# Performance work log

Hardware: AMD Instinct MI355X
Metric: run time of the kernel (lower is better)

Reference implementation:

```python
import jax, jax.numpy as jnp
import numpy as np

HIDDEN = 128
EDGE_DIM = 64
N_NODES = 50000
N_EDGES = 600000

def _linear_params(key, fan_in, fan_out):
    kw, kb = jax.random.split(key)
    bound = 1.0 / np.sqrt(fan_in)
    W = jax.random.uniform(kw, (fan_in, fan_out), minval=-bound, maxval=bound, dtype=jnp.float32)
    b = jax.random.uniform(kb, (fan_out,), minval=-bound, maxval=bound, dtype=jnp.float32)
    return W, b

def setup_inputs() -> dict:
    key = jax.random.key(0)
    ks = jax.random.split(key, 10)
    h = jax.random.normal(ks[0], (N_NODES, HIDDEN), dtype=jnp.float32)
    edge_index = jax.random.randint(ks[1], (2, N_EDGES), 0, N_NODES, dtype=jnp.int64)
    edge_attr = jax.random.normal(ks[2], (N_EDGES, EDGE_DIM), dtype=jnp.float32)
    mW1, mb1 = _linear_params(ks[3], 2 * HIDDEN + EDGE_DIM, HIDDEN)
    mW2, mb2 = _linear_params(ks[4], HIDDEN, HIDDEN)
    mW3, mb3 = _linear_params(ks[5], HIDDEN, HIDDEN)
    uW1, ub1 = _linear_params(ks[6], 2 * HIDDEN, HIDDEN)
    uW2, ub2 = _linear_params(ks[7], HIDDEN, HIDDEN)
    gamma = jnp.ones((HIDDEN,), dtype=jnp.float32)
    beta = jnp.zeros((HIDDEN,), dtype=jnp.float32)
    return {"h": h, "edge_index": edge_index, "edge_attr": edge_attr,
            "mW1": mW1, "mb1": mb1, "mW2": mW2, "mb2": mb2, "mW3": mW3, "mb3": mb3,
            "uW1": uW1, "ub1": ub1, "uW2": uW2, "ub2": ub2,
            "gamma": gamma, "beta": beta}

def reference(h, edge_index, edge_attr, mW1, mb1, mW2, mb2, mW3, mb3, uW1, ub1, uW2, ub2, gamma, beta):
    src, dst = edge_index[0], edge_index[1]
    # message MLP on [E, 2*H + edge_dim]
    x = jnp.concatenate([h[src], h[dst], edge_attr], axis=-1)
    x = jax.nn.gelu(x @ mW1 + mb1)
    x = jax.nn.gelu(x @ mW2 + mb2)
    msgs = x @ mW3 + mb3  # [E, H]
    # scatter-mean aggregate to destination nodes
    agg = jax.ops.segment_sum(msgs, dst, num_segments=h.shape[0])
    count = jax.ops.segment_sum(jnp.ones((dst.shape[0], 1), dtype=h.dtype), dst, num_segments=h.shape[0])
    agg = agg / (count + 1e-8)
    # update MLP
    u = jnp.concatenate([h, agg], axis=-1)
    u = jax.nn.gelu(u @ uW1 + ub1)
    out = u @ uW2 + ub2
    # LayerNorm(out + h)
    y = out + h
    mu = jnp.mean(y, axis=-1, keepdims=True)
    var = jnp.var(y, axis=-1, keepdims=True)
    return (y - mu) / jnp.sqrt(var + 1e-5) * gamma + beta
```

## Files before the change

kernel.cpp:

```cpp
#include <hip/hip_runtime.h>

#define E_TOTAL 600000
#define NN 50000

typedef _Float16 half8 __attribute__((ext_vector_type(8)));
typedef _Float16 half2v __attribute__((ext_vector_type(2)));
typedef float float4v __attribute__((ext_vector_type(4)));
typedef float float2v __attribute__((ext_vector_type(2)));

__device__ __forceinline__ float gelu_tanh(float x) {
    const float A = 1.5957691216057308f;
    const float B = 0.0713548163f;
    float z = x * __builtin_fmaf(B, x * x, A);
    float ex = __expf(z);
    float r = __builtin_amdgcn_rcpf(ex + 1.0f);
    return __builtin_fmaf(-x, r, x);
}

__device__ __forceinline__ int act_idx(int c, int row, int q) {
    int idx = ((c * 128 + row) << 3) + q;
    idx ^= ((row >> 3) & 3) << 4;
    idx ^= (c & 1) << 3;
    return idx;
}
__device__ __forceinline__ int act_idx64(int c, int row, int q) {
    int idx = ((c * 64 + row) << 3) + q;
    idx ^= ((row >> 3) & 3) << 4;
    idx ^= (c & 1) << 3;
    return idx;
}

__device__ __forceinline__ half8 cvt8(float4v x0, float4v x1) {
    half8 a;
    a[0] = (_Float16)x0[0]; a[1] = (_Float16)x0[1]; a[2] = (_Float16)x0[2]; a[3] = (_Float16)x0[3];
    a[4] = (_Float16)x1[0]; a[5] = (_Float16)x1[1]; a[6] = (_Float16)x1[2]; a[7] = (_Float16)x1[3];
    return a;
}

__global__ __launch_bounds__(256) void prep_kernel(
    const float* __restrict__ mW1, const float* __restrict__ mW2, const float* __restrict__ mW3,
    const float* __restrict__ uW1, const float* __restrict__ uW2,
    const float* __restrict__ h,
    _Float16* __restrict__ pw, _Float16* __restrict__ hf)
{
    const int stride = gridDim.x * 256;
    for (int t = blockIdx.x * 256 + threadIdx.x; t < 922880; t += stride) {
        if (t < 122880) {
            const float* src;
            int loc;
            if (t < 40960)        { src = mW1; loc = t; }
            else if (t < 57344)   { src = mW2; loc = t - 40960; }
            else if (t < 73728)   { src = mW3; loc = t - 57344; }
            else if (t < 106496)  { src = uW1; loc = t - 73728; }
            else                  { src = uW2; loc = t - 106496; }
            int i   = loc & 7;
            int col = (loc >> 3) & 127;
            int c   = loc >> 10;
            pw[t] = (_Float16)src[(8 * c + i) * 128 + col];
        } else {
            int i = t - 122880;
            float4v a = ((const float4v*)h)[2 * i];
            float4v b = ((const float4v*)h)[2 * i + 1];
            ((half8*)hf)[i] = cvt8(a, b);
        }
    }
}

__device__ __forceinline__ int detect_i64(const int* ei) {
    int allz = 1;
    #pragma unroll
    for (int j = 1; j < 64; j += 2) allz &= (ei[j] == 0);
    return allz;
}

__global__ __launch_bounds__(256) void count_kernel(const int* __restrict__ ei, int* __restrict__ cnt_i) {
    __shared__ int s_mode;
    if (threadIdx.x == 0) s_mode = detect_i64(ei);
    __syncthreads();
    int e = blockIdx.x * 256 + threadIdx.x;
    if (e >= E_TOTAL) return;
    int d = s_mode ? (int)((const long long*)ei)[E_TOTAL + e] : ei[E_TOTAL + e];
    atomicAdd(&cnt_i[d], 1);
}

__global__ __launch_bounds__(1024) void scan_kernel(const int* __restrict__ cnt_i, int* __restrict__ offs) {
    __shared__ int part[1024];
    const int t = threadIdx.x;
    const int PER = (NN + 1023) / 1024;
    const int base = t * PER;
    int s = 0;
    for (int j = 0; j < PER; ++j) { int idx = base + j; if (idx < NN) s += cnt_i[idx]; }
    part[t] = s;
    __syncthreads();
    for (int off = 1; off < 1024; off <<= 1) {
        int v = (t >= off) ? part[t - off] : 0;
        __syncthreads();
        part[t] += v;
        __syncthreads();
    }
    int run = (t == 0) ? 0 : part[t - 1];
    for (int j = 0; j < PER; ++j) { int idx = base + j; if (idx < NN) { offs[idx] = run; run += cnt_i[idx]; } }
    if (t == 1023) offs[NN] = part[1023];
}

__global__ __launch_bounds__(256) void fill_kernel(const int* __restrict__ ei, const int* __restrict__ offs,
                                                   int* __restrict__ cursor, int* __restrict__ perm) {
    __shared__ int s_mode;
    if (threadIdx.x == 0) s_mode = detect_i64(ei);
    __syncthreads();
    int e = blockIdx.x * 256 + threadIdx.x;
    if (e >= E_TOTAL) return;
    int d = s_mode ? (int)((const long long*)ei)[E_TOTAL + e] : ei[E_TOTAL + e];
    int pos = offs[d] + atomicAdd(&cursor[d], 1);
    perm[pos] = e;
}

template<int ATOMIC>
__global__ __launch_bounds__(128, 3) void msg_kernel(
    const _Float16* __restrict__ hf16, const int* __restrict__ ei, const float* __restrict__ eattr,
    const int* __restrict__ perm,
    const _Float16* __restrict__ pw1, const _Float16* __restrict__ pw2, const _Float16* __restrict__ pw3,
    const float* __restrict__ mb1, const float* __restrict__ mb2, const float* __restrict__ mb3,
    _Float16* __restrict__ msgs, float* __restrict__ agg, float* __restrict__ cnt)
{
    __shared__ int s_e[64];
    __shared__ int s_src[64];
    __shared__ int s_dst[64];
    __shared__ int s_mode;
    __shared__ __align__(16) _Float16 s_act[16 * 64 * 8];

    const int tid = threadIdx.x;
    const int e0  = blockIdx.x * 64;

    if (tid == 0) s_mode = detect_i64(ei);
    __syncthreads();

    if (tid < 64) {
        int e = perm[e0 + tid];
        s_e[tid] = e;
        int srcn, dstn;
        if (s_mode) {
            const long long* e64 = (const long long*)ei;
            srcn = (int)e64[e];
            dstn = (int)e64[E_TOTAL + e];
        } else {
            srcn = ei[e];
            dstn = ei[E_TOTAL + e];
        }
        s_src[tid] = srcn;
        s_dst[tid] = dstn;
        if (ATOMIC) unsafeAtomicAdd(&cnt[dstn], 1.0f);
    }
    __syncthreads();

    const int w = tid >> 6, l = tid & 63, lhi = l >> 4, llo = l & 15;
    const int r0 = 32 * w;
    const float4v fzero = {0.0f, 0.0f, 0.0f, 0.0f};

    const _Float16* srcP[2];
    const _Float16* dstP[2];
    const float*    eP[2];
    #pragma unroll
    for (int ms = 0; ms < 2; ++ms) {
        const int row = r0 + 16 * ms + llo;
        srcP[ms] = hf16 + (size_t)s_src[row] * 128 + 8 * lhi;
        dstP[ms] = hf16 + (size_t)s_dst[row] * 128 + 8 * lhi;
        eP[ms]   = eattr + (size_t)s_e[row] * 64 + 8 * lhi;
    }

    float4v acc[2][8];
    #pragma unroll
    for (int ms = 0; ms < 2; ++ms)
        #pragma unroll
        for (int t = 0; t < 8; ++t) acc[ms][t] = fzero;

    half8 af[4][2];
    #pragma unroll
    for (int s = 0; s < 4; ++s)
        #pragma unroll
        for (int ms = 0; ms < 2; ++ms)
            af[s][ms] = *(const half8*)(srcP[ms] + 32 * s);

    #pragma unroll
    for (int s = 0; s < 10; ++s) {
        const int bbase = ((4 * s + lhi) * 128 + llo) << 3;
        #pragma unroll
        for (int t = 0; t < 8; ++t) {
            const half8 b = *(const half8*)(pw1 + bbase + (t << 7));
            acc[0][t] = __builtin_amdgcn_mfma_f32_16x16x32_f16(af[s & 3][0], b, acc[0][t], 0, 0, 0);
            acc[1][t] = __builtin_amdgcn_mfma_f32_16x16x32_f16(af[s & 3][1], b, acc[1][t], 0, 0, 0);
        }
        if (s + 4 <= 9) {
            const int sn = s + 4;
            #pragma unroll
            for (int ms = 0; ms < 2; ++ms) {
                if (sn < 8) {
                    af[sn & 3][ms] = *(const half8*)(dstP[ms] + 32 * (sn - 4));
                } else {
                    const float* p = eP[ms] + 32 * (sn - 8);
                    float4v x0 = *(const float4v*)p;
                    float4v x1 = *(const float4v*)(p + 4);
                    af[sn & 3][ms] = cvt8(x0, x1);
                }
            }
        }
    }

    #pragma unroll
    for (int t = 0; t < 8; ++t) {
        const int col = 16 * t + llo;
        const float b1 = mb1[col];
        #pragma unroll
        for (int ms = 0; ms < 2; ++ms)
            #pragma unroll
            for (int i = 0; i < 4; ++i) {
                const int row = r0 + 16 * ms + 4 * lhi + i;
                float v = gelu_tanh(acc[ms][t][i] + b1);
                s_act[act_idx64(col >> 3, row, col & 7)] = (_Float16)v;
            }
    }

    float4v acc2[2][8];
    #pragma unroll
    for (int ms = 0; ms < 2; ++ms)
        #pragma unroll
        for (int t = 0; t < 8; ++t) acc2[ms][t] = fzero;

    #pragma unroll
    for (int s = 0; s < 4; ++s) {
        half8 a2[2];
        #pragma unroll
        for (int ms = 0; ms < 2; ++ms)
            a2[ms] = *(const half8*)&s_act[act_idx64(4 * s + lhi, r0 + 16 * ms + llo, 0)];
        const int bbase = ((4 * s + lhi) * 128 + llo) << 3;
        #pragma unroll
        for (int t = 0; t < 8; ++t) {
            const half8 b = *(const half8*)(pw2 + bbase + (t << 7));
            acc2[0][t] = __builtin_amdgcn_mfma_f32_16x16x32_f16(a2[0], b, acc2[0][t], 0, 0, 0);
            acc2[1][t] = __builtin_amdgcn_mfma_f32_16x16x32_f16(a2[1], b, acc2[1][t], 0, 0, 0);
        }
    }

    #pragma unroll
    for (int t = 0; t < 8; ++t) {
        const int col = 16 * t + llo;
        const float b2 = mb2[col];
        #pragma unroll
        for (int ms = 0; ms < 2; ++ms)
            #pragma unroll
            for (int i = 0; i < 4; ++i) {
                const int row = r0 + 16 * ms + 4 * lhi + i;
                float v = gelu_tanh(acc2[ms][t][i] + b2);
                s_act[act_idx64(col >> 3, row, col & 7)] = (_Float16)v;
            }
    }

    float4v acc3[2][8];
    #pragma unroll
    for (int ms = 0; ms < 2; ++ms)
        #pragma unroll
        for (int t = 0; t < 8; ++t) acc3[ms][t] = fzero;

    #pragma unroll
    for (int s = 0; s < 4; ++s) {
        half8 a3[2];
        #pragma unroll
        for (int ms = 0; ms < 2; ++ms)
            a3[ms] = *(const half8*)&s_act[act_idx64(4 * s + lhi, r0 + 16 * ms + llo, 0)];
        const int bbase = ((4 * s + lhi) * 128 + llo) << 3;
        #pragma unroll
        for (int t = 0; t < 8; ++t) {
            const half8 b = *(const half8*)(pw3 + bbase + (t << 7));
            acc3[0][t] = __builtin_amdgcn_mfma_f32_16x16x32_f16(a3[0], b, acc3[0][t], 0, 0, 0);
            acc3[1][t] = __builtin_amdgcn_mfma_f32_16x16x32_f16(a3[1], b, acc3[1][t], 0, 0, 0);
        }
    }

    float mb3v[8];
    #pragma unroll
    for (int t = 0; t < 8; ++t) mb3v[t] = mb3[16 * t + llo];

    #pragma unroll
    for (int ms = 0; ms < 2; ++ms)
        #pragma unroll
        for (int i = 0; i < 4; ++i) {
            const int row = r0 + 16 * ms + 4 * lhi + i;
            if (ATOMIC) {
                const size_t dbase = (size_t)s_dst[row] * 128;
                #pragma unroll
                for (int t = 0; t < 8; ++t)
                    unsafeAtomicAdd(&agg[dbase + 16 * t + llo], acc3[ms][t][i] + mb3v[t]);
            } else {
                _Float16* mrow = msgs + (size_t)(e0 + row) * 128;
                #pragma unroll
                for (int t = 0; t < 8; ++t)
                    __builtin_nontemporal_store((_Float16)(acc3[ms][t][i] + mb3v[t]), mrow + 16 * t + llo);
            }
        }
}

template<int FUSED>
__global__ __launch_bounds__(256) void upd_kernel(
    const float* __restrict__ h, const _Float16* __restrict__ hf16,
    const _Float16* __restrict__ msgs, const int* __restrict__ offs,
    const _Float16* __restrict__ pu1, const _Float16* __restrict__ pu2,
    const float* __restrict__ ub1, const float* __restrict__ ub2,
    const float* __restrict__ gamma, const float* __restrict__ beta,
    const float* __restrict__ agg, const float* __restrict__ cnt,
    float* __restrict__ out)
{
    __shared__ __align__(16) _Float16 s_act[16 * 128 * 8];

    const int tid = threadIdx.x;
    const int n0  = blockIdx.x * 128;
    const int w = tid >> 6, l = tid & 63, lhi = l >> 4, llo = l & 15;
    const int r0 = 32 * w;
    const float4v fzero = {0.0f, 0.0f, 0.0f, 0.0f};

    float rcp[2];
    size_t nodeOff[2];
    int beg[2], end[2];
    #pragma unroll
    for (int ms = 0; ms < 2; ++ms) {
        int node = n0 + r0 + 16 * ms + llo;
        if (node >= NN) node = NN - 1;
        nodeOff[ms] = (size_t)node * 128;
        if (FUSED) {
            beg[ms] = offs[node]; end[ms] = offs[node + 1];
            rcp[ms] = 1.0f / ((float)(end[ms] - beg[ms]) + 1e-8f);
        } else {
            rcp[ms] = 1.0f / (cnt[node] + 1e-8f);
        }
    }

    half8 afA[2][4];
    if (FUSED) {
        #pragma unroll
        for (int ms = 0; ms < 2; ++ms) {
            float msum[4][8];
            #pragma unroll
            for (int s = 0; s < 4; ++s)
                #pragma unroll
                for (int j = 0; j < 8; ++j) msum[s][j] = 0.0f;
            for (int r = beg[ms]; r < end[ms]; ++r) {
                const half8* rp = (const half8*)(msgs + (size_t)r * 128) + lhi;
                #pragma unroll
                for (int s = 0; s < 4; ++s) {
                    half8 v = __builtin_nontemporal_load(rp + 4 * s);
                    #pragma unroll
                    for (int j = 0; j < 8; ++j) msum[s][j] += (float)v[j];
                }
            }
            #pragma unroll
            for (int s = 0; s < 4; ++s) {
                half8 a;
                #pragma unroll
                for (int j = 0; j < 8; ++j) a[j] = (_Float16)(msum[s][j] * rcp[ms]);
                afA[ms][s] = a;
            }
        }
    }

    float4v acc[2][8];
    #pragma unroll
    for (int ms = 0; ms < 2; ++ms)
        #pragma unroll
        for (int t = 0; t < 8; ++t) acc[ms][t] = fzero;

    #pragma unroll
    for (int s = 0; s < 8; ++s) {
        half8 af[2];
        #pragma unroll
        for (int ms = 0; ms < 2; ++ms) {
            if (s < 4) {
                af[ms] = *(const half8*)(hf16 + nodeOff[ms] + 32 * s + 8 * lhi);
            } else if (FUSED) {
                af[ms] = afA[ms][s - 4];
            } else {
                const float* p = agg + nodeOff[ms] + 32 * (s - 4) + 8 * lhi;
                float4v x0 = *(const float4v*)p;
                float4v x1 = *(const float4v*)(p + 4);
                x0 *= rcp[ms]; x1 *= rcp[ms];
                af[ms] = cvt8(x0, x1);
            }
        }
        const int bbase = ((4 * s + lhi) * 128 + llo) << 3;
        #pragma unroll
        for (int t = 0; t < 8; ++t) {
            const half8 b = *(const half8*)(pu1 + bbase + (t << 7));
            acc[0][t] = __builtin_amdgcn_mfma_f32_16x16x32_f16(af[0], b, acc[0][t], 0, 0, 0);
            acc[1][t] = __builtin_amdgcn_mfma_f32_16x16x32_f16(af[1], b, acc[1][t], 0, 0, 0);
        }
    }

    #pragma unroll
    for (int t = 0; t < 8; ++t) {
        const int col = 16 * t + llo;
        const float b1 = ub1[col];
        #pragma unroll
        for (int ms = 0; ms < 2; ++ms)
            #pragma unroll
            for (int i = 0; i < 4; ++i) {
                const int row = r0 + 16 * ms + 4 * lhi + i;
                float v = gelu_tanh(acc[ms][t][i] + b1);
                s_act[act_idx(col >> 3, row, col & 7)] = (_Float16)v;
            }
    }

    float4v acc2[2][8];
    #pragma unroll
    for (int ms = 0; ms < 2; ++ms)
        #pragma unroll
        for (int t = 0; t < 8; ++t) acc2[ms][t] = fzero;

    #pragma unroll
    for (int s = 0; s < 4; ++s) {
        half8 af[2];
        #pragma unroll
        for (int ms = 0; ms < 2; ++ms)
            af[ms] = *(const half8*)&s_act[act_idx(4 * s + lhi, r0 + 16 * ms + llo, 0)];
        const int bbase = ((4 * s + lhi) * 128 + llo) << 3;
        #pragma unroll
        for (int t = 0; t < 8; ++t) {
            const half8 b = *(const half8*)(pu2 + bbase + (t << 7));
            acc2[0][t] = __builtin_amdgcn_mfma_f32_16x16x32_f16(af[0], b, acc2[0][t], 0, 0, 0);
            acc2[1][t] = __builtin_amdgcn_mfma_f32_16x16x32_f16(af[1], b, acc2[1][t], 0, 0, 0);
        }
    }

    float ub2v[8], gv[8], bv[8];
    #pragma unroll
    for (int t = 0; t < 8; ++t) {
        const int col = 16 * t + llo;
        ub2v[t] = ub2[col]; gv[t] = gamma[col]; bv[t] = beta[col];
    }

    #pragma unroll
    for (int ms = 0; ms < 2; ++ms)
        #pragma unroll
        for (int i = 0; i < 4; ++i) {
            const int noderow = n0 + r0 + 16 * ms + 4 * lhi + i;
            const int nodec = noderow < NN ? noderow : NN - 1;
            float y[8];
            float sum = 0.0f;
            #pragma unroll
            for (int t = 0; t < 8; ++t) {
                const int col = 16 * t + llo;
                float v = acc2[ms][t][i] + ub2v[t] + h[(size_t)nodec * 128 + col];
                y[t] = v; sum += v;
            }
            sum += __shfl_xor(sum, 1, 16);
            sum += __shfl_xor(sum, 2, 16);
            sum += __shfl_xor(sum, 4, 16);
            sum += __shfl_xor(sum, 8, 16);
            const float mu = sum * (1.0f / 128.0f);
            float sq = 0.0f;
            #pragma unroll
            for (int t = 0; t < 8; ++t) { float d = y[t] - mu; sq += d * d; }
            sq += __shfl_xor(sq, 1, 16);
            sq += __shfl_xor(sq, 2, 16);
            sq += __shfl_xor(sq, 4, 16);
            sq += __shfl_xor(sq, 8, 16);
            const float rs = rsqrtf(sq * (1.0f / 128.0f) + 1e-5f);
            if (noderow < NN) {
                #pragma unroll
                for (int t = 0; t < 8; ++t) {
                    const int col = 16 * t + llo;
                    out[(size_t)noderow * 128 + col] = (y[t] - mu) * rs * gv[t] + bv[t];
                }
            }
        }
}

extern "C" void kernel_launch(void* const* d_in, const int* in_sizes, int n_in,
                              void* d_out, int out_size, void* d_ws, size_t ws_size,
                              hipStream_t stream) {
    const float* h     = (const float*)d_in[0];
    const int*   ei    = (const int*)d_in[1];
    const float* eattr = (const float*)d_in[2];
    const float* mW1   = (const float*)d_in[3];
    const float* mb1   = (const float*)d_in[4];
    const float* mW2   = (const float*)d_in[5];
    const float* mb2   = (const float*)d_in[6];
    const float* mW3   = (const float*)d_in[7];
    const float* mb3   = (const float*)d_in[8];
    const float* uW1   = (const float*)d_in[9];
    const float* ub1   = (const float*)d_in[10];
    const float* uW2   = (const float*)d_in[11];
    const float* ub2   = (const float*)d_in[12];
    const float* gamma = (const float*)d_in[13];
    const float* beta  = (const float*)d_in[14];
    float* out = (float*)d_out;

    char* ws = (char*)d_ws;

    const size_t OFF_MSGS = 0;
    const size_t OFF_HF   = 153600000;
    const size_t OFF_CNTI = 166400000;
    const size_t OFF_CURS = 166600000;
    const size_t OFF_OFFS = 166800000;
    const size_t OFF_PERM = 167000064;
    const size_t OFF_PW   = 169400064;
    const size_t NEED     = 169645824;

    if (ws_size >= NEED) {
        _Float16* msgs  = (_Float16*)(ws + OFF_MSGS);
        _Float16* hf16  = (_Float16*)(ws + OFF_HF);
        int* cnt_i      = (int*)(ws + OFF_CNTI);
        int* cursor     = (int*)(ws + OFF_CURS);
        int* offs       = (int*)(ws + OFF_OFFS);
        int* perm       = (int*)(ws + OFF_PERM);
        _Float16* pw    = (_Float16*)(ws + OFF_PW);
        _Float16* pw1 = pw;
        _Float16* pw2 = pw + 40960;
        _Float16* pw3 = pw + 57344;
        _Float16* pu1 = pw + 73728;
        _Float16* pu2 = pw + 106496;

        hipMemsetAsync(ws + OFF_CNTI, 0, 400000, stream);

        count_kernel<<<(E_TOTAL + 255) / 256, 256, 0, stream>>>(ei, cnt_i);
        scan_kernel<<<1, 1024, 0, stream>>>(cnt_i, offs);
        fill_kernel<<<(E_TOTAL + 255) / 256, 256, 0, stream>>>(ei, offs, cursor, perm);
        prep_kernel<<<1024, 256, 0, stream>>>(mW1, mW2, mW3, uW1, uW2, h, pw, hf16);

        msg_kernel<0><<<E_TOTAL / 64, 128, 0, stream>>>(
            hf16, ei, eattr, perm, pw1, pw2, pw3, mb1, mb2, mb3, msgs, nullptr, nullptr);

        upd_kernel<1><<<(NN + 127) / 128, 256, 0, stream>>>(
            h, hf16, msgs, offs, pu1, pu2, ub1, ub2, gamma, beta, nullptr, nullptr, out);
    } else {
        float* agg     = (float*)ws;
        float* cnt     = (float*)(ws + 25600000);
        _Float16* hf16 = (_Float16*)(ws + 25800000);
        int* cnt_i     = (int*)(ws + 38600000);
        int* cursor    = (int*)(ws + 38800000);
        int* offs      = (int*)(ws + 39000000);
        int* perm      = (int*)(ws + 39200064);
        _Float16* pw   = (_Float16*)(ws + 41600064);
        _Float16* pw1 = pw;
        _Float16* pw2 = pw + 40960;
        _Float16* pw3 = pw + 57344;
        _Float16* pu1 = pw + 73728;
        _Float16* pu2 = pw + 106496;

        hipMemsetAsync(ws, 0, 25800000, stream);
        hipMemsetAsync(ws + 38600000, 0, 400000, stream);

        count_kernel<<<(E_TOTAL + 255) / 256, 256, 0, stream>>>(ei, cnt_i);
        scan_kernel<<<1, 1024, 0, stream>>>(cnt_i, offs);
        fill_kernel<<<(E_TOTAL + 255) / 256, 256, 0, stream>>>(ei, offs, cursor, perm);
        prep_kernel<<<1024, 256, 0, stream>>>(mW1, mW2, mW3, uW1, uW2, h, pw, hf16);

        msg_kernel<1><<<E_TOTAL / 64, 128, 0, stream>>>(
            hf16, ei, eattr, perm, pw1, pw2, pw3, mb1, mb2, mb3, nullptr, agg, cnt);

        upd_kernel<0><<<(NN + 127) / 128, 256, 0, stream>>>(
            h, hf16, nullptr, nullptr, pu1, pu2, ub1, ub2, gamma, beta, agg, cnt, out);
    }
}
```

Measured before the change: 716.6 us.

## Process edges in natural order, scatter messages by rank, add separate aggregation kernel

The message kernel now reads edges in their original order, so edge_attr and edge_index loads are contiguous instead of gathered through a permutation. Each message row is written to its CSR-sorted slot using a rank array built by the fill kernel. A new aggregation kernel, one wavefront per node, sums each node's contiguous message rows into an fp16 mean buffer. The update kernel then just loads that buffer, which removes the serial per-lane reduction loop and its load imbalance. This costs an extra launch and an extra round-trip of the aggregate buffer, and the message stores become scattered. The fallback path drops the unused CSR build.

```diff
diff --git a/kernel.cpp b/kernel.cpp
--- a/kernel.cpp
+++ b/kernel.cpp
@@ -104,7 +104,7 @@
 }
 
 __global__ __launch_bounds__(256) void fill_kernel(const int* __restrict__ ei, const int* __restrict__ offs,
-                                                   int* __restrict__ cursor, int* __restrict__ perm) {
+                                                   int* __restrict__ cursor, int* __restrict__ rank) {
     __shared__ int s_mode;
     if (threadIdx.x == 0) s_mode = detect_i64(ei);
     __syncthreads();
@@ -112,20 +112,46 @@
     if (e >= E_TOTAL) return;
     int d = s_mode ? (int)((const long long*)ei)[E_TOTAL + e] : ei[E_TOTAL + e];
     int pos = offs[d] + atomicAdd(&cursor[d], 1);
-    perm[pos] = e;
+    rank[e] = pos;
+}
+
+__global__ __launch_bounds__(256) void agg_kernel(const _Float16* __restrict__ msgs,
+                                                  const int* __restrict__ offs,
+                                                  _Float16* __restrict__ aggf) {
+    const int node = blockIdx.x * 4 + (threadIdx.x >> 6);
+    const int l = threadIdx.x & 63;
+    const int beg = offs[node], end = offs[node + 1];
+    float2v s = {0.0f, 0.0f};
+    const half2v* p = (const half2v*)msgs + (size_t)beg * 64 + l;
+    int j = beg;
+    for (; j + 3 < end; j += 4, p += 256) {
+        half2v a = __builtin_nontemporal_load(p);
+        half2v b = __builtin_nontemporal_load(p + 64);
+        half2v c = __builtin_nontemporal_load(p + 128);
+        half2v d = __builtin_nontemporal_load(p + 192);
+        s.x += (float)a[0] + (float)b[0] + (float)c[0] + (float)d[0];
+        s.y += (float)a[1] + (float)b[1] + (float)c[1] + (float)d[1];
+    }
+    for (; j < end; ++j, p += 64) {
+        half2v v = __builtin_nontemporal_load(p);
+        s.x += (float)v[0]; s.y += (float)v[1];
+    }
+    const float rcp = 1.0f / ((float)(end - beg) + 1e-8f);
+    half2v o; o[0] = (_Float16)(s.x * rcp); o[1] = (_Float16)(s.y * rcp);
+    ((half2v*)aggf)[(size_t)node * 64 + l] = o;
 }
 
 template<int ATOMIC>
 __global__ __launch_bounds__(128, 3) void msg_kernel(
     const _Float16* __restrict__ hf16, const int* __restrict__ ei, const float* __restrict__ eattr,
-    const int* __restrict__ perm,
+    const int* __restrict__ rank,
     const _Float16* __restrict__ pw1, const _Float16* __restrict__ pw2, const _Float16* __restrict__ pw3,
     const float* __restrict__ mb1, const float* __restrict__ mb2, const float* __restrict__ mb3,
     _Float16* __restrict__ msgs, float* __restrict__ agg, float* __restrict__ cnt)
 {
-    __shared__ int s_e[64];
     __shared__ int s_src[64];
     __shared__ int s_dst[64];
+    __shared__ int s_rk[64];
     __shared__ int s_mode;
     __shared__ __align__(16) _Float16 s_act[16 * 64 * 8];
 
@@ -136,8 +162,7 @@
     __syncthreads();
 
     if (tid < 64) {
-        int e = perm[e0 + tid];
-        s_e[tid] = e;
+        int e = e0 + tid;
         int srcn, dstn;
         if (s_mode) {
             const long long* e64 = (const long long*)ei;
@@ -149,7 +174,11 @@
         }
         s_src[tid] = srcn;
         s_dst[tid] = dstn;
-        if (ATOMIC) unsafeAtomicAdd(&cnt[dstn], 1.0f);
+        if (ATOMIC) {
+            unsafeAtomicAdd(&cnt[dstn], 1.0f);
+        } else {
+            s_rk[tid] = rank[e];
+        }
     }
     __syncthreads();
 
@@ -165,7 +194,7 @@
         const int row = r0 + 16 * ms + llo;
         srcP[ms] = hf16 + (size_t)s_src[row] * 128 + 8 * lhi;
         dstP[ms] = hf16 + (size_t)s_dst[row] * 128 + 8 * lhi;
-        eP[ms]   = eattr + (size_t)s_e[row] * 64 + 8 * lhi;
+        eP[ms]   = eattr + (size_t)(e0 + row) * 64 + 8 * lhi;
     }
 
     float4v acc[2][8];
@@ -291,7 +320,7 @@
                 for (int t = 0; t < 8; ++t)
                     unsafeAtomicAdd(&agg[dbase + 16 * t + llo], acc3[ms][t][i] + mb3v[t]);
             } else {
-                _Float16* mrow = msgs + (size_t)(e0 + row) * 128;
+                _Float16* mrow = msgs + (size_t)s_rk[row] * 128;
                 #pragma unroll
                 for (int t = 0; t < 8; ++t)
                     __builtin_nontemporal_store((_Float16)(acc3[ms][t][i] + mb3v[t]), mrow + 16 * t + llo);
@@ -299,10 +328,10 @@
         }
 }
 
-template<int FUSED>
+template<int AGGF16>
 __global__ __launch_bounds__(256) void upd_kernel(
     const float* __restrict__ h, const _Float16* __restrict__ hf16,
-    const _Float16* __restrict__ msgs, const int* __restrict__ offs,
+    const _Float16* __restrict__ aggf,
     const _Float16* __restrict__ pu1, const _Float16* __restrict__ pu2,
     const float* __restrict__ ub1, const float* __restrict__ ub2,
     const float* __restrict__ gamma, const float* __restrict__ beta,
@@ -319,46 +348,12 @@
 
     float rcp[2];
     size_t nodeOff[2];
-    int beg[2], end[2];
     #pragma unroll
     for (int ms = 0; ms < 2; ++ms) {
         int node = n0 + r0 + 16 * ms + llo;
         if (node >= NN) node = NN - 1;
         nodeOff[ms] = (size_t)node * 128;
-        if (FUSED) {
-            beg[ms] = offs[node]; end[ms] = offs[node + 1];
-            rcp[ms] = 1.0f / ((float)(end[ms] - beg[ms]) + 1e-8f);
-        } else {
-            rcp[ms] = 1.0f / (cnt[node] + 1e-8f);
-        }
-    }
-
-    half8 afA[2][4];
-    if (FUSED) {
-        #pragma unroll
-        for (int ms = 0; ms < 2; ++ms) {
-            float msum[4][8];
-            #pragma unroll
-            for (int s = 0; s < 4; ++s)
-                #pragma unroll
-                for (int j = 0; j < 8; ++j) msum[s][j] = 0.0f;
-            for (int r = beg[ms]; r < end[ms]; ++r) {
-                const half8* rp = (const half8*)(msgs + (size_t)r * 128) + lhi;
-                #pragma unroll
-                for (int s = 0; s < 4; ++s) {
-                    half8 v = __builtin_nontemporal_load(rp + 4 * s);
-                    #pragma unroll
-                    for (int j = 0; j < 8; ++j) msum[s][j] += (float)v[j];
-                }
-            }
-            #pragma unroll
-            for (int s = 0; s < 4; ++s) {
-                half8 a;
-                #pragma unroll
-                for (int j = 0; j < 8; ++j) a[j] = (_Float16)(msum[s][j] * rcp[ms]);
-                afA[ms][s] = a;
-            }
-        }
+        if (!AGGF16) rcp[ms] = 1.0f / (cnt[node] + 1e-8f);
     }
 
     float4v acc[2][8];
@@ -374,8 +369,8 @@
         for (int ms = 0; ms < 2; ++ms) {
             if (s < 4) {
                 af[ms] = *(const half8*)(hf16 + nodeOff[ms] + 32 * s + 8 * lhi);
-            } else if (FUSED) {
-                af[ms] = afA[ms][s - 4];
+            } else if (AGGF16) {
+                af[ms] = *(const half8*)(aggf + nodeOff[ms] + 32 * (s - 4) + 8 * lhi);
             } else {
                 const float* p = agg + nodeOff[ms] + 32 * (s - 4) + 8 * lhi;
                 float4v x0 = *(const float4v*)p;
@@ -496,20 +491,22 @@
 
     const size_t OFF_MSGS = 0;
     const size_t OFF_HF   = 153600000;
-    const size_t OFF_CNTI = 166400000;
-    const size_t OFF_CURS = 166600000;
-    const size_t OFF_OFFS = 166800000;
-    const size_t OFF_PERM = 167000064;
-    const size_t OFF_PW   = 169400064;
-    const size_t NEED     = 169645824;
+    const size_t OFF_AGG  = 166400000;
+    const size_t OFF_CNTI = 179200000;
+    const size_t OFF_CURS = 179400000;
+    const size_t OFF_OFFS = 179600000;
+    const size_t OFF_RANK = 179800064;
+    const size_t OFF_PW   = 182200064;
+    const size_t NEED     = 182445824;
 
     if (ws_size >= NEED) {
         _Float16* msgs  = (_Float16*)(ws + OFF_MSGS);
         _Float16* hf16  = (_Float16*)(ws + OFF_HF);
+        _Float16* aggf  = (_Float16*)(ws + OFF_AGG);
         int* cnt_i      = (int*)(ws + OFF_CNTI);
         int* cursor     = (int*)(ws + OFF_CURS);
         int* offs       = (int*)(ws + OFF_OFFS);
-        int* perm       = (int*)(ws + OFF_PERM);
+        int* rank       = (int*)(ws + OFF_RANK);
         _Float16* pw    = (_Float16*)(ws + OFF_PW);
         _Float16* pw1 = pw;
         _Float16* pw2 = pw + 40960;
@@ -521,23 +518,21 @@
 
         count_kernel<<<(E_TOTAL + 255) / 256, 256, 0, stream>>>(ei, cnt_i);
         scan_kernel<<<1, 1024, 0, stream>>>(cnt_i, offs);
-        fill_kernel<<<(E_TOTAL + 255) / 256, 256, 0, stream>>>(ei, offs, cursor, perm);
+        fill_kernel<<<(E_TOTAL + 255) / 256, 256, 0, stream>>>(ei, offs, cursor, rank);
         prep_kernel<<<1024, 256, 0, stream>>>(mW1, mW2, mW3, uW1, uW2, h, pw, hf16);
 
         msg_kernel<0><<<E_TOTAL / 64, 128, 0, stream>>>(
-            hf16, ei, eattr, perm, pw1, pw2, pw3, mb1, mb2, mb3, msgs, nullptr, nullptr);
+            hf16, ei, eattr, rank, pw1, pw2, pw3, mb1, mb2, mb3, msgs, nullptr, nullptr);
+
+        agg_kernel<<<NN / 4, 256, 0, stream>>>(msgs, offs, aggf);
 
         upd_kernel<1><<<(NN + 127) / 128, 256, 0, stream>>>(
-            h, hf16, msgs, offs, pu1, pu2, ub1, ub2, gamma, beta, nullptr, nullptr, out);
+            h, hf16, aggf, pu1, pu2, ub1, ub2, gamma, beta, nullptr, nullptr, out);
     } else {
         float* agg     = (float*)ws;
         float* cnt     = (float*)(ws + 25600000);
         _Float16* hf16 = (_Float16*)(ws + 25800000);
-        int* cnt_i     = (int*)(ws + 38600000);
-        int* cursor    = (int*)(ws + 38800000);
-        int* offs      = (int*)(ws + 39000000);
-        int* perm      = (int*)(ws + 39200064);
-        _Float16* pw   = (_Float16*)(ws + 41600064);
+        _Float16* pw   = (_Float16*)(ws + 38600000);
         _Float16* pw1 = pw;
         _Float16* pw2 = pw + 40960;
         _Float16* pw3 = pw + 57344;
@@ -545,17 +540,13 @@
         _Float16* pu2 = pw + 106496;
 
         hipMemsetAsync(ws, 0, 25800000, stream);
-        hipMemsetAsync(ws + 38600000, 0, 400000, stream);
-
-        count_kernel<<<(E_TOTAL + 255) / 256, 256, 0, stream>>>(ei, cnt_i);
-        scan_kernel<<<1, 1024, 0, stream>>>(cnt_i, offs);
-        fill_kernel<<<(E_TOTAL + 255) / 256, 256, 0, stream>>>(ei, offs, cursor, perm);
+
         prep_kernel<<<1024, 256, 0, stream>>>(mW1, mW2, mW3, uW1, uW2, h, pw, hf16);
 
         msg_kernel<1><<<E_TOTAL / 64, 128, 0, stream>>>(
-            hf16, ei, eattr, perm, pw1, pw2, pw3, mb1, mb2, mb3, nullptr, agg, cnt);
+            hf16, ei, eattr, nullptr, pw1, pw2, pw3, mb1, mb2, mb3, nullptr, agg, cnt);
 
         upd_kernel<0><<<(NN + 127) / 128, 256, 0, stream>>>(
-            h, hf16, nullptr, nullptr, pu1, pu2, ub1, ub2, gamma, beta, agg, cnt, out);
-    }
-}
+            h, hf16, nullptr, pu1, pu2, ub1, ub2, gamma, beta, agg, cnt, out);
+    }
+}
```

Measured after the change: 690.2 us. 3.7% less time.
